# Kernel tuning notes

Measured on AMD Instinct MI355X. Metric: run time of the kernel, lower is better.

## Reference

```python
import jax, jax.numpy as jnp
import numpy as np


def setup_inputs() -> dict:
    key = jax.random.key(0)
    k1, k2 = jax.random.split(key)
    B, C, H, W = 1, 256, 96, 96
    C8 = C // 8
    x = jax.random.normal(k1, (B, C, H, W), dtype=jnp.float32)
    # 1x1 conv == per-pixel linear projection; weight [C8, C], bias [C8]
    w_conv = jax.random.normal(k2, (C8, C), dtype=jnp.float32) * (1.0 / np.sqrt(C))
    b_conv = jnp.zeros((C8,), dtype=jnp.float32)
    return {"x": x, "w_conv": w_conv, "b_conv": b_conv}


def reference(x, w_conv, b_conv):
    B, C, H, W = x.shape  # B must be 1 (module constraint)
    C8 = w_conv.shape[0]
    # conv_1: 1x1 conv -> [B, C8, H, W]
    x1 = jnp.einsum('bchw,oc->bohw', x, w_conv) + b_conv[None, :, None, None]
    x1 = x1.reshape(-1, H, W)                      # [C8, H, W] (B=1)
    x2 = x1.transpose(2, 1, 0).reshape(-1, C8)     # [W*H, C8], row idx = w*H + h
    x3 = x1.transpose(0, 2, 1).reshape(-1, W * H)  # [C8, W*H], col idx = w*H + h
    x4 = jax.nn.softmax(x2 @ x3, axis=-1)          # [W*H, W*H]
    x5 = x.reshape(-1, W * H)                      # [C, W*H], col idx = h*W + w
    x6 = jax.nn.softmax(x5 @ x4, axis=-1)          # [C, W*H]
    x7 = x6.reshape(B, C, H, W)
    return jax.nn.softmax(x7 + x, axis=-1)         # softmax over W
```

## Files before the change

### kernel.cpp

```cpp
#include <hip/hip_runtime.h>
#include <math.h>

#define HW 9216
#define NI 18
#define PROW 72

typedef __attribute__((ext_vector_type(8))) short bf16x8;
typedef __attribute__((ext_vector_type(4))) float f32x4;
typedef unsigned short ushort_t;
typedef unsigned int uint_t;

__device__ __forceinline__ ushort_t f2bf(float f) {
    union { float f; uint_t u; } v; v.f = f;
    uint_t u = v.u + 0x7FFF + ((v.u >> 16) & 1);
    return (ushort_t)(u >> 16);
}

__device__ __forceinline__ uint_t cvtpk_bf16(float lo, float hi) {
    uint_t r;
    asm("v_cvt_pk_bf16_f32 %0, %1, %2" : "=v"(r) : "v"(lo), "v"(hi));
    return r;
}

__device__ __forceinline__ float pexp(float s, float mu) {
    return exp2f(fmaf(s, 1.44269504f, mu));
}

__global__ __launch_bounds__(256) void k1_conv(
        const float* __restrict__ x, const float* __restrict__ wc,
        const float* __restrict__ bc, ushort_t* __restrict__ Gbt,
        ushort_t* __restrict__ xtile) {
    __shared__ float wt[256][32];
    __shared__ float red[8][32][33];
    int t = threadIdx.x;
    int jt = blockIdx.x;
    for (int i = t; i < 256 * 32; i += 256) {
        int o = i >> 8, c = i & 255;
        wt[c][o] = wc[i];
    }
    __syncthreads();
    int px = t & 31, cg = t >> 5;
    int n = jt * 32 + px;
    float acc[32];
    #pragma unroll
    for (int o = 0; o < 32; ++o) acc[o] = 0.f;
    int c0 = cg * 32;
    ushort_t* xt_out = &xtile[(size_t)jt * 8192 + px];
    for (int cc = 0; cc < 32; ++cc) {
        int c = c0 + cc;
        float xv = x[c * HW + n];
        xt_out[c * 32] = f2bf(xv);
        #pragma unroll
        for (int o4 = 0; o4 < 8; ++o4) {
            float4 wv = *(const float4*)&wt[c][o4 * 4];
            acc[o4*4+0] = fmaf(wv.x, xv, acc[o4*4+0]);
            acc[o4*4+1] = fmaf(wv.y, xv, acc[o4*4+1]);
            acc[o4*4+2] = fmaf(wv.z, xv, acc[o4*4+2]);
            acc[o4*4+3] = fmaf(wv.w, xv, acc[o4*4+3]);
        }
    }
    #pragma unroll
    for (int o = 0; o < 32; ++o) red[cg][px][o] = acc[o];
    __syncthreads();
    int px2 = t >> 3, o2 = (t & 7) * 4;
    float s[4] = {0.f, 0.f, 0.f, 0.f};
    #pragma unroll
    for (int g = 0; g < 8; ++g) {
        s[0] += red[g][px2][o2 + 0];
        s[1] += red[g][px2][o2 + 1];
        s[2] += red[g][px2][o2 + 2];
        s[3] += red[g][px2][o2 + 3];
    }
    int n2 = jt * 32 + px2;
    int h = n2 / 96, w = n2 % 96;
    int p = w * 96 + h;
    uint2 pk;
    pk.x = (uint_t)f2bf(s[0] + bc[o2+0]) | ((uint_t)f2bf(s[1] + bc[o2+1]) << 16);
    pk.y = (uint_t)f2bf(s[2] + bc[o2+2]) | ((uint_t)f2bf(s[3] + bc[o2+3]) << 16);
    *(uint2*)&Gbt[p * 32 + o2] = pk;
}

__global__ __launch_bounds__(512) void k2_stats(
        const ushort_t* __restrict__ Gbt, float* __restrict__ m_part,
        float* __restrict__ l_part) {
    __shared__ float mred[2][64], lred[2][64];
    int t = threadIdx.x;
    int w = t >> 6, l = t & 63;
    int l15 = l & 15, lg = l >> 4;
    int jb = blockIdx.x % 144, qs = blockIdx.x / 144;
    int j0 = jb * 64;
    int rf = w & 3, qp = w >> 2;
    bf16x8 aj = *(const bf16x8*)&Gbt[(j0 + rf * 16 + l15) * 32 + lg * 8];
    float m[4], lsum[4];
    #pragma unroll
    for (int r = 0; r < 4; ++r) { m[r] = -INFINITY; lsum[r] = 0.f; }
    int qbeg = qs * 1152;
    for (int tq = 0; tq < 18; ++tq) {
        int q0 = qbeg + tq * 64;
        bf16x8 b0 = *(const bf16x8*)&Gbt[(q0 + qp * 32 + l15) * 32 + lg * 8];
        bf16x8 b1 = *(const bf16x8*)&Gbt[(q0 + qp * 32 + 16 + l15) * 32 + lg * 8];
        f32x4 s0 = {0.f,0.f,0.f,0.f}, s1 = {0.f,0.f,0.f,0.f};
        s0 = __builtin_amdgcn_mfma_f32_16x16x32_bf16(aj, b0, s0, 0, 0, 0);
        s1 = __builtin_amdgcn_mfma_f32_16x16x32_bf16(aj, b1, s1, 0, 0, 0);
        #pragma unroll
        for (int r = 0; r < 4; ++r) {
            float tm = fmaxf(s0[r], s1[r]);
            float nm = fmaxf(m[r], tm);
            lsum[r] = lsum[r] * __expf(m[r] - nm)
                    + __expf(s0[r] - nm) + __expf(s1[r] - nm);
            m[r] = nm;
        }
    }
    #pragma unroll
    for (int off = 1; off < 16; off <<= 1) {
        #pragma unroll
        for (int r = 0; r < 4; ++r) {
            float mo = __shfl_xor(m[r], off);
            float lo = __shfl_xor(lsum[r], off);
            float nm = fmaxf(m[r], mo);
            lsum[r] = lsum[r] * __expf(m[r] - nm) + lo * __expf(mo - nm);
            m[r] = nm;
        }
    }
    if (l15 == 0) {
        #pragma unroll
        for (int r = 0; r < 4; ++r) {
            mred[qp][rf * 16 + lg * 4 + r] = m[r];
            lred[qp][rf * 16 + lg * 4 + r] = lsum[r];
        }
    }
    __syncthreads();
    if (t < 64) {
        float m0 = mred[0][t], m1 = mred[1][t];
        float l0 = lred[0][t], l1 = lred[1][t];
        float nm = fmaxf(m0, m1);
        float lv = l0 * __expf(m0 - nm) + l1 * __expf(m1 - nm);
        m_part[qs * HW + j0 + t] = nm;
        l_part[qs * HW + j0 + t] = lv;
    }
}

__global__ __launch_bounds__(256) void k2b_merge(
        const float* __restrict__ m_part, const float* __restrict__ l_part,
        float* __restrict__ muS) {
    int j = blockIdx.x * 256 + threadIdx.x;
    float nm = -INFINITY;
    #pragma unroll
    for (int s = 0; s < 8; ++s) nm = fmaxf(nm, m_part[s * HW + j]);
    float lv = 0.f;
    #pragma unroll
    for (int s = 0; s < 8; ++s)
        lv += l_part[s * HW + j] * __expf(m_part[s * HW + j] - nm);
    muS[j] = -(nm + logf(lv)) * 1.44269504f;
}

__global__ __launch_bounds__(256, 4) void k3_pv(
        const ushort_t* __restrict__ xtile, const ushort_t* __restrict__ Gbt,
        const float* __restrict__ muS, float* __restrict__ Z) {
    __shared__ ushort_t Pw[4][32][PROW];
    const int t = threadIdx.x;
    const int w = t >> 6;
    const int l15 = t & 15, lg = (t >> 4) & 3;
    const int qb = blockIdx.x % 288, ps = blockIdx.x / 288;
    const int q0 = qb * 32;
    const int cbase = w * 64;

    bf16x8 bq0 = *(const bf16x8*)&Gbt[(q0 + l15) * 32 + lg * 8];
    bf16x8 bq1 = *(const bf16x8*)&Gbt[(q0 + 16 + l15) * 32 + lg * 8];

    f32x4 acc[4][2];
    #pragma unroll
    for (int ci = 0; ci < 4; ++ci) {
        acc[ci][0] = (f32x4){0.f,0.f,0.f,0.f};
        acc[ci][1] = (f32x4){0.f,0.f,0.f,0.f};
    }

    const int p0beg = ps * (NI * 64);
    const int tile0 = ps * (NI * 2);
    ushort_t* pw = &Pw[w][0][0];

    bf16x8 ap[4];
    #pragma unroll
    for (int pm = 0; pm < 4; ++pm)
        ap[pm] = *(const bf16x8*)&Gbt[(p0beg + pm * 16 + l15) * 32 + lg * 8];

    for (int it = 0; it < NI; ++it) {
        const int p0 = p0beg + it * 64;
        const ushort_t* xa =
            &xtile[((size_t)(tile0 + 2 * it) * 256 + cbase + l15) * 32 + lg * 8];
        bf16x8 a0[4];
        #pragma unroll
        for (int ci = 0; ci < 4; ++ci)
            a0[ci] = *(const bf16x8*)&xa[ci * 512];

        f32x4 s[4][2];
        #pragma unroll
        for (int pm = 0; pm < 4; ++pm) {
            f32x4 z = {0.f,0.f,0.f,0.f};
            s[pm][0] = __builtin_amdgcn_mfma_f32_16x16x32_bf16(ap[pm], bq0, z, 0,0,0);
            s[pm][1] = __builtin_amdgcn_mfma_f32_16x16x32_bf16(ap[pm], bq1, z, 0,0,0);
        }
        if (it < NI - 1) {
            const int pn = p0 + 64;
            #pragma unroll
            for (int pm = 0; pm < 4; ++pm)
                ap[pm] = *(const bf16x8*)&Gbt[(pn + pm * 16 + l15) * 32 + lg * 8];
        }
        #pragma unroll
        for (int pm = 0; pm < 4; ++pm) {
            float4 mu = *(const float4*)&muS[p0 + pm * 16 + lg * 4];
            #pragma unroll
            for (int qn = 0; qn < 2; ++qn) {
                uint2 u;
                u.x = cvtpk_bf16(pexp(s[pm][qn][0], mu.x),
                                 pexp(s[pm][qn][1], mu.y));
                u.y = cvtpk_bf16(pexp(s[pm][qn][2], mu.z),
                                 pexp(s[pm][qn][3], mu.w));
                *(uint2*)&pw[(qn * 16 + l15) * PROW + pm * 16 + lg * 4] = u;
            }
        }
        bf16x8 a1[4];
        const ushort_t* xa1 = xa + 8192;
        #pragma unroll
        for (int ci = 0; ci < 4; ++ci)
            a1[ci] = *(const bf16x8*)&xa1[ci * 512];

        bf16x8 b00 = *(const bf16x8*)&pw[l15 * PROW + lg * 8];
        bf16x8 b01 = *(const bf16x8*)&pw[(16 + l15) * PROW + lg * 8];
        #pragma unroll
        for (int ci = 0; ci < 4; ++ci) {
            acc[ci][0] = __builtin_amdgcn_mfma_f32_16x16x32_bf16(a0[ci], b00, acc[ci][0], 0,0,0);
            acc[ci][1] = __builtin_amdgcn_mfma_f32_16x16x32_bf16(a0[ci], b01, acc[ci][1], 0,0,0);
        }
        bf16x8 b10 = *(const bf16x8*)&pw[l15 * PROW + 32 + lg * 8];
        bf16x8 b11 = *(const bf16x8*)&pw[(16 + l15) * PROW + 32 + lg * 8];
        #pragma unroll
        for (int ci = 0; ci < 4; ++ci) {
            acc[ci][0] = __builtin_amdgcn_mfma_f32_16x16x32_bf16(a1[ci], b10, acc[ci][0], 0,0,0);
            acc[ci][1] = __builtin_amdgcn_mfma_f32_16x16x32_bf16(a1[ci], b11, acc[ci][1], 0,0,0);
        }
    }
    const int qc0 = q0 + l15;
    #pragma unroll
    for (int ci = 0; ci < 4; ++ci) {
        const int crow = cbase + ci * 16 + lg * 4;
        #pragma unroll
        for (int r = 0; r < 4; ++r) {
            float* zr = &Z[(size_t)(crow + r) * HW + qc0];
            atomicAdd(zr,      acc[ci][0][r]);
            atomicAdd(zr + 16, acc[ci][1][r]);
        }
    }
}

__global__ __launch_bounds__(512) void k4_softmax(
        const float* __restrict__ x, float* __restrict__ ZO) {
    __shared__ float zrow[HW];
    __shared__ float red[8];
    int t = threadIdx.x, c = blockIdx.x;
    int lane = t & 63, wid = t >> 6;
    const float* Zr = &ZO[(size_t)c * HW];
    float lm = -INFINITY;
    #pragma unroll
    for (int k = 0; k < 18; ++k) {
        float v = Zr[t + 512 * k];
        zrow[t + 512 * k] = v;
        lm = fmaxf(lm, v);
    }
    #pragma unroll
    for (int off = 32; off; off >>= 1) lm = fmaxf(lm, __shfl_xor(lm, off));
    if (lane == 0) red[wid] = lm;
    __syncthreads();
    float M = fmaxf(fmaxf(fmaxf(red[0], red[1]), fmaxf(red[2], red[3])),
                    fmaxf(fmaxf(red[4], red[5]), fmaxf(red[6], red[7])));
    __syncthreads();
    float ls = 0.f;
    #pragma unroll
    for (int k = 0; k < 18; ++k) {
        int i = t + 512 * k;
        float e = __expf(zrow[i] - M);
        zrow[i] = e;
        ls += e;
    }
    #pragma unroll
    for (int off = 32; off; off >>= 1) ls += __shfl_xor(ls, off);
    if (lane == 0) red[wid] = ls;
    __syncthreads();
    float rS = 1.0f / (red[0] + red[1] + red[2] + red[3]
                     + red[4] + red[5] + red[6] + red[7]);
    const float* xr = &x[(size_t)c * HW];
    float* outr = &ZO[(size_t)c * HW];
    for (int kk = 0; kk < 12; ++kk) {
        int h = wid + kk * 8;
        int base = h * 96;
        float v0 = fmaf(zrow[base + lane], rS, xr[base + lane]);
        float v1 = (lane < 32)
                 ? fmaf(zrow[base + 64 + lane], rS, xr[base + 64 + lane])
                 : -INFINITY;
        float mm = fmaxf(v0, v1);
        #pragma unroll
        for (int off = 32; off; off >>= 1) mm = fmaxf(mm, __shfl_xor(mm, off));
        float e0 = __expf(v0 - mm);
        float e1 = (lane < 32) ? __expf(v1 - mm) : 0.f;
        float ss = e0 + e1;
        #pragma unroll
        for (int off = 32; off; off >>= 1) ss += __shfl_xor(ss, off);
        float r = 1.0f / ss;
        outr[base + lane] = e0 * r;
        if (lane < 32) outr[base + 64 + lane] = e1 * r;
    }
}

extern "C" void kernel_launch(void* const* d_in, const int* in_sizes, int n_in,
                              void* d_out, int out_size, void* d_ws, size_t ws_size,
                              hipStream_t stream) {
    const float* x  = (const float*)d_in[0];
    const float* wc = (const float*)d_in[1];
    const float* bc = (const float*)d_in[2];
    float* Z = (float*)d_out;

    float* m_part = (float*)d_ws;
    float* l_part = m_part + 8 * HW;
    float* muS    = l_part + 8 * HW;
    ushort_t* xtile = (ushort_t*)(muS + HW);
    ushort_t* Gbt   = xtile + 256 * HW;

    k1_conv   <<<288,  256, 0, stream>>>(x, wc, bc, Gbt, xtile);
    k2_stats  <<<1152, 512, 0, stream>>>(Gbt, m_part, l_part);
    k2b_merge <<<36,   256, 0, stream>>>(m_part, l_part, muS);
    hipMemsetAsync(Z, 0, (size_t)out_size * sizeof(float), stream);
    k3_pv     <<<2304, 256, 0, stream>>>(xtile, Gbt, muS, Z);
    k4_softmax<<<256,  512, 0, stream>>>(x, Z);
}
```

Measured before the change: 237.5 us.

## Materialize softmax probability matrix to global memory and split PV into two kernels

When the workspace is large enough, the fused score/exp/PV kernel is replaced by two kernels. The first computes the full 9216x9216 bf16 probability matrix P into global memory. The second runs a plain MFMA GEMM of x against P with atomic accumulation into Z. This removes the shared-memory round trip and the per-iteration exp work from the PV loop, but adds roughly 170 MB of global writes and reads. If the workspace is too small, the old fused path is kept as a fallback.

```diff
diff --git a/kernel.cpp b/kernel.cpp
--- a/kernel.cpp
+++ b/kernel.cpp
@@ -154,6 +154,98 @@
     muS[j] = -(nm + logf(lv)) * 1.44269504f;
 }
 
+__global__ __launch_bounds__(256) void kP(
+        const ushort_t* __restrict__ Gbt, const float* __restrict__ muS,
+        ushort_t* __restrict__ Pt) {
+    const int t = threadIdx.x;
+    const int w = t >> 6;
+    const int l15 = t & 15, lg = (t >> 4) & 3;
+    const int pb = blockIdx.x / 72, qb = blockIdx.x % 72;
+    const int p0 = pb * 64;
+    const int q0 = qb * 128 + w * 32;
+    bf16x8 bq0 = *(const bf16x8*)&Gbt[(q0 + l15) * 32 + lg * 8];
+    bf16x8 bq1 = *(const bf16x8*)&Gbt[(q0 + 16 + l15) * 32 + lg * 8];
+    bf16x8 ap[4];
+    #pragma unroll
+    for (int pm = 0; pm < 4; ++pm)
+        ap[pm] = *(const bf16x8*)&Gbt[(p0 + pm * 16 + l15) * 32 + lg * 8];
+    #pragma unroll
+    for (int pm = 0; pm < 4; ++pm) {
+        f32x4 z = {0.f,0.f,0.f,0.f};
+        f32x4 s0 = __builtin_amdgcn_mfma_f32_16x16x32_bf16(ap[pm], bq0, z, 0,0,0);
+        f32x4 s1 = __builtin_amdgcn_mfma_f32_16x16x32_bf16(ap[pm], bq1, z, 0,0,0);
+        const int pcol = p0 + pm * 16 + lg * 4;
+        float4 mu = *(const float4*)&muS[pcol];
+        uint2 u0, u1;
+        u0.x = cvtpk_bf16(pexp(s0[0], mu.x), pexp(s0[1], mu.y));
+        u0.y = cvtpk_bf16(pexp(s0[2], mu.z), pexp(s0[3], mu.w));
+        u1.x = cvtpk_bf16(pexp(s1[0], mu.x), pexp(s1[1], mu.y));
+        u1.y = cvtpk_bf16(pexp(s1[2], mu.z), pexp(s1[3], mu.w));
+        *(uint2*)&Pt[(size_t)(q0 + l15) * HW + pcol]      = u0;
+        *(uint2*)&Pt[(size_t)(q0 + 16 + l15) * HW + pcol] = u1;
+    }
+}
+
+__global__ __launch_bounds__(256) void k3g(
+        const ushort_t* __restrict__ xtile, const ushort_t* __restrict__ Pt,
+        float* __restrict__ Z) {
+    const int t = threadIdx.x;
+    const int w = t >> 6;
+    const int l15 = t & 15, lg = (t >> 4) & 3;
+    const int qb = blockIdx.x % 144, ps = blockIdx.x / 144;
+    const int q0 = qb * 64;
+    const int cbase = w * 64;
+    f32x4 acc[4][4];
+    #pragma unroll
+    for (int ci = 0; ci < 4; ++ci)
+        #pragma unroll
+        for (int qn = 0; qn < 4; ++qn) acc[ci][qn] = (f32x4){0.f,0.f,0.f,0.f};
+    const int tile0 = ps * 36;
+    const size_t prow0 = (size_t)(q0 + l15) * HW;
+
+    for (int it = 0; it < 36; ++it) {
+        const int p = ps * 1152 + it * 32;
+        const ushort_t* xa =
+            &xtile[((size_t)(tile0 + it) * 256 + cbase + l15) * 32 + lg * 8];
+        bf16x8 a0 = *(const bf16x8*)&xa[0];
+        bf16x8 a1 = *(const bf16x8*)&xa[512];
+        bf16x8 a2 = *(const bf16x8*)&xa[1024];
+        bf16x8 a3 = *(const bf16x8*)&xa[1536];
+        const ushort_t* pb = &Pt[prow0 + p + lg * 8];
+        bf16x8 b0 = *(const bf16x8*)&pb[0];
+        bf16x8 b1 = *(const bf16x8*)&pb[16 * HW];
+        bf16x8 b2 = *(const bf16x8*)&pb[32 * HW];
+        bf16x8 b3 = *(const bf16x8*)&pb[48 * HW];
+        acc[0][0] = __builtin_amdgcn_mfma_f32_16x16x32_bf16(a0, b0, acc[0][0], 0,0,0);
+        acc[1][0] = __builtin_amdgcn_mfma_f32_16x16x32_bf16(a1, b0, acc[1][0], 0,0,0);
+        acc[2][0] = __builtin_amdgcn_mfma_f32_16x16x32_bf16(a2, b0, acc[2][0], 0,0,0);
+        acc[3][0] = __builtin_amdgcn_mfma_f32_16x16x32_bf16(a3, b0, acc[3][0], 0,0,0);
+        acc[0][1] = __builtin_amdgcn_mfma_f32_16x16x32_bf16(a0, b1, acc[0][1], 0,0,0);
+        acc[1][1] = __builtin_amdgcn_mfma_f32_16x16x32_bf16(a1, b1, acc[1][1], 0,0,0);
+        acc[2][1] = __builtin_amdgcn_mfma_f32_16x16x32_bf16(a2, b1, acc[2][1], 0,0,0);
+        acc[3][1] = __builtin_amdgcn_mfma_f32_16x16x32_bf16(a3, b1, acc[3][1], 0,0,0);
+        acc[0][2] = __builtin_amdgcn_mfma_f32_16x16x32_bf16(a0, b2, acc[0][2], 0,0,0);
+        acc[1][2] = __builtin_amdgcn_mfma_f32_16x16x32_bf16(a1, b2, acc[1][2], 0,0,0);
+        acc[2][2] = __builtin_amdgcn_mfma_f32_16x16x32_bf16(a2, b2, acc[2][2], 0,0,0);
+        acc[3][2] = __builtin_amdgcn_mfma_f32_16x16x32_bf16(a3, b2, acc[3][2], 0,0,0);
+        acc[0][3] = __builtin_amdgcn_mfma_f32_16x16x32_bf16(a0, b3, acc[0][3], 0,0,0);
+        acc[1][3] = __builtin_amdgcn_mfma_f32_16x16x32_bf16(a1, b3, acc[1][3], 0,0,0);
+        acc[2][3] = __builtin_amdgcn_mfma_f32_16x16x32_bf16(a2, b3, acc[2][3], 0,0,0);
+        acc[3][3] = __builtin_amdgcn_mfma_f32_16x16x32_bf16(a3, b3, acc[3][3], 0,0,0);
+    }
+    #pragma unroll
+    for (int ci = 0; ci < 4; ++ci) {
+        const int crow = cbase + ci * 16 + lg * 4;
+        #pragma unroll
+        for (int r = 0; r < 4; ++r) {
+            float* zr = &Z[(size_t)(crow + r) * HW + q0 + l15];
+            #pragma unroll
+            for (int qn = 0; qn < 4; ++qn)
+                atomicAdd(zr + qn * 16, acc[ci][qn][r]);
+        }
+    }
+}
+
 __global__ __launch_bounds__(256, 4) void k3_pv(
         const ushort_t* __restrict__ xtile, const ushort_t* __restrict__ Gbt,
         const float* __restrict__ muS, float* __restrict__ Z) {
@@ -164,21 +256,17 @@
     const int qb = blockIdx.x % 288, ps = blockIdx.x / 288;
     const int q0 = qb * 32;
     const int cbase = w * 64;
-
     bf16x8 bq0 = *(const bf16x8*)&Gbt[(q0 + l15) * 32 + lg * 8];
     bf16x8 bq1 = *(const bf16x8*)&Gbt[(q0 + 16 + l15) * 32 + lg * 8];
-
     f32x4 acc[4][2];
     #pragma unroll
     for (int ci = 0; ci < 4; ++ci) {
         acc[ci][0] = (f32x4){0.f,0.f,0.f,0.f};
         acc[ci][1] = (f32x4){0.f,0.f,0.f,0.f};
     }
-
     const int p0beg = ps * (NI * 64);
     const int tile0 = ps * (NI * 2);
     ushort_t* pw = &Pw[w][0][0];
-
     bf16x8 ap[4];
     #pragma unroll
     for (int pm = 0; pm < 4; ++pm)
@@ -192,7 +280,6 @@
         #pragma unroll
         for (int ci = 0; ci < 4; ++ci)
             a0[ci] = *(const bf16x8*)&xa[ci * 512];
-
         f32x4 s[4][2];
         #pragma unroll
         for (int pm = 0; pm < 4; ++pm) {
@@ -224,7 +311,6 @@
         #pragma unroll
         for (int ci = 0; ci < 4; ++ci)
             a1[ci] = *(const bf16x8*)&xa1[ci * 512];
-
         bf16x8 b00 = *(const bf16x8*)&pw[l15 * PROW + lg * 8];
         bf16x8 b01 = *(const bf16x8*)&pw[(16 + l15) * PROW + lg * 8];
         #pragma unroll
@@ -324,11 +410,21 @@
     float* muS    = l_part + 8 * HW;
     ushort_t* xtile = (ushort_t*)(muS + HW);
     ushort_t* Gbt   = xtile + 256 * HW;
+    ushort_t* Pt    = Gbt + 32 * HW;
+
+    const size_t need = 17u * HW * sizeof(float)
+                      + ((size_t)256 * HW + 32u * HW + (size_t)HW * HW)
+                        * sizeof(ushort_t);
 
     k1_conv   <<<288,  256, 0, stream>>>(x, wc, bc, Gbt, xtile);
     k2_stats  <<<1152, 512, 0, stream>>>(Gbt, m_part, l_part);
     k2b_merge <<<36,   256, 0, stream>>>(m_part, l_part, muS);
     hipMemsetAsync(Z, 0, (size_t)out_size * sizeof(float), stream);
-    k3_pv     <<<2304, 256, 0, stream>>>(xtile, Gbt, muS, Z);
-    k4_softmax<<<256,  512, 0, stream>>>(x, Z);
-}
+    if (ws_size >= need) {
+        kP  <<<10368, 256, 0, stream>>>(Gbt, muS, Pt);
+        k3g <<<1152,  256, 0, stream>>>(xtile, Pt, Z);
+    } else {
+        k3_pv <<<2304, 256, 0, stream>>>(xtile, Gbt, muS, Z);
+    }
+    k4_softmax<<<256, 512, 0, stream>>>(x, Z);
+}
```

New measurement: 284.1 us. 1.2x slower.
